# Optimization experiments

Measured on AMD Instinct MI355X. Metric: run time of the kernel, lower is better.

## Reference

```python
import jax, jax.numpy as jnp
import numpy as np

B, HEADS, SCALES, POINTS, HIDDEN = 1, 8, 4, 4, 192
HEAD_DIM = HIDDEN // HEADS
OFFSET_SCALE = 0.35
EPS = 1e-5


def conv1x1(x, W, b=None):
    # x: [B,C,D,H,W], W: [O,C]
    y = jnp.einsum('bcdhw,oc->bodhw', x, W)
    if b is not None:
        y = y + b[None, :, None, None, None]
    return y


def base_grid(D, H, W, dtype):
    z = jnp.linspace(-1.0, 1.0, D, dtype=dtype)
    y = jnp.linspace(-1.0, 1.0, H, dtype=dtype)
    x = jnp.linspace(-1.0, 1.0, W, dtype=dtype)
    zz, yy, xx = jnp.meshgrid(z, y, x, indexing='ij')
    return jnp.stack((xx, yy, zz), axis=-1)  # [D,H,W,3] (x,y,z order)


def trilinear_sample(val, grid):
    # val: [BH,C,Dv,Hv,Wv]; grid: [BH,N,3] normalized (x,y,z), align_corners=False, border padding
    BH, C, Dv, Hv, Wv = val.shape
    unnorm = lambda g, s: jnp.clip(((g + 1.0) * s - 1.0) * 0.5, 0.0, s - 1.0)
    ix = unnorm(grid[..., 0], Wv)
    iy = unnorm(grid[..., 1], Hv)
    iz = unnorm(grid[..., 2], Dv)
    x0f, y0f, z0f = jnp.floor(ix), jnp.floor(iy), jnp.floor(iz)
    wx, wy, wz = ix - x0f, iy - y0f, iz - z0f
    x0 = x0f.astype(jnp.int32); x1 = jnp.minimum(x0 + 1, Wv - 1)
    y0 = y0f.astype(jnp.int32); y1 = jnp.minimum(y0 + 1, Hv - 1)
    z0 = z0f.astype(jnp.int32); z1 = jnp.minimum(z0 + 1, Dv - 1)
    vflat = val.reshape(BH, C, Dv * Hv * Wv)
    gather = jax.vmap(lambda v, i: v[:, i])  # -> [BH,C,N]
    def corner(zi, yi, xi):
        return gather(vflat, (zi * Hv + yi) * Wv + xi)
    w = lambda a: a[:, None, :]  # broadcast weight over channel dim
    out = (corner(z0, y0, x0) * w((1 - wz) * (1 - wy) * (1 - wx))
           + corner(z0, y0, x1) * w((1 - wz) * (1 - wy) * wx)
           + corner(z0, y1, x0) * w((1 - wz) * wy * (1 - wx))
           + corner(z0, y1, x1) * w((1 - wz) * wy * wx)
           + corner(z1, y0, x0) * w(wz * (1 - wy) * (1 - wx))
           + corner(z1, y0, x1) * w(wz * (1 - wy) * wx)
           + corner(z1, y1, x0) * w(wz * wy * (1 - wx))
           + corner(z1, y1, x1) * w(wz * wy * wx))
    return out


def fsad_forward(query_feature, values, Wq, Wvs, Woff, boff, Wwt, bwt, Wout, gamma, beta):
    Bq, _, D, H, W = query_feature.shape
    N = D * H * W
    q = conv1x1(query_feature, Wq)
    off = conv1x1(q, Woff, boff).reshape(Bq, HEADS, SCALES, POINTS, 3, D, H, W)
    off = jnp.tanh(off) * OFFSET_SCALE
    aw = conv1x1(q, Wwt, bwt).reshape(Bq, HEADS, SCALES * POINTS, D, H, W)
    aw = jax.nn.softmax(aw, axis=2).reshape(Bq, HEADS, SCALES, POINTS, D, H, W)
    bg = base_grid(D, H, W, q.dtype)  # [D,H,W,3]
    acc = jnp.zeros((Bq, HEADS, HEAD_DIM, D, H, W), q.dtype)
    for s in range(SCALES):
        feat = values[s]
        val = conv1x1(feat, Wvs[s]).reshape(Bq * HEADS, HEAD_DIM, *feat.shape[2:])
        # off[:,:,s]: [B,Hh,P,3,D,H,W] -> grid [B,Hh,P,D,H,W,3]
        grid = bg[None, None, None] + jnp.moveaxis(off[:, :, s], 3, -1)
        grid = grid.reshape(Bq * HEADS, POINTS * N, 3)
        sampled = trilinear_sample(val, grid).reshape(Bq, HEADS, HEAD_DIM, POINTS, D, H, W)
        acc = acc + jnp.einsum('bhcpdyx,bhpdyx->bhcdyx', sampled, aw[:, :, s])
    out = conv1x1(acc.reshape(Bq, HIDDEN, D, H, W), Wout)
    # InstanceNorm3d(affine=True)
    mu = out.mean(axis=(2, 3, 4), keepdims=True)
    var = out.var(axis=(2, 3, 4), keepdims=True)
    out = (out - mu) * jax.lax.rsqrt(var + EPS)
    return out * gamma[None, :, None, None, None] + beta[None, :, None, None, None]


def setup_inputs() -> dict:
    key = jax.random.key(0)
    ks = jax.random.split(key, 16)
    value_channels = [32, 64, 128, 256]
    sizes = [64, 32, 16, 8]
    inp = {
        'query_feature': jax.random.normal(ks[0], (1, 128, 16, 16, 16), jnp.float32),
        'v0': jax.random.normal(ks[1], (1, 32, 64, 64, 64), jnp.float32),
        'v1': jax.random.normal(ks[2], (1, 64, 32, 32, 32), jnp.float32),
        'v2': jax.random.normal(ks[3], (1, 128, 16, 16, 16), jnp.float32),
        'v3': jax.random.normal(ks[4], (1, 256, 8, 8, 8), jnp.float32),
        'Wq': jax.random.normal(ks[5], (HIDDEN, 128), jnp.float32) * 0.05,
        'Wv0': jax.random.normal(ks[6], (HIDDEN, 32), jnp.float32) * 0.05,
        'Wv1': jax.random.normal(ks[7], (HIDDEN, 64), jnp.float32) * 0.05,
        'Wv2': jax.random.normal(ks[8], (HIDDEN, 128), jnp.float32) * 0.05,
        'Wv3': jax.random.normal(ks[9], (HIDDEN, 256), jnp.float32) * 0.05,
        'Woff': jax.random.normal(ks[10], (HEADS * SCALES * POINTS * 3, HIDDEN), jnp.float32) * 0.05,
        'boff': jnp.zeros((HEADS * SCALES * POINTS * 3,), jnp.float32),
        'Wwt': jax.random.normal(ks[11], (HEADS * SCALES * POINTS, HIDDEN), jnp.float32) * 0.05,
        'bwt': jnp.zeros((HEADS * SCALES * POINTS,), jnp.float32),
        'Wout': jax.random.normal(ks[12], (128, HIDDEN), jnp.float32) * 0.05,
        'gamma': jnp.ones((128,), jnp.float32),
        'beta': jnp.zeros((128,), jnp.float32),
    }
    return inp


def reference(query_feature, v0, v1, v2, v3, Wq, Wv0, Wv1, Wv2, Wv3, Woff, boff, Wwt, bwt, Wout, gamma, beta):
    return fsad_forward(query_feature, [v0, v1, v2, v3], Wq, [Wv0, Wv1, Wv2, Wv3], Woff, boff, Wwt, bwt, Wout, gamma, beta)
```

## Files before the change

### kernel.cpp

```cpp
#include <hip/hip_runtime.h>
#include <hip/hip_fp16.h>
#include <cmath>

#define N_Q 4096
#define HEADS 8
#define HEAD_DIM 24
#define HIDDEN 192

__device__ __forceinline__ float4 ld4(const float* p) { return *(const float4*)p; }

__device__ __forceinline__ void fma8h(float* u, float w, const __half* p) {
    uint4 raw = *(const uint4*)p;
    const __half2* h2 = reinterpret_cast<const __half2*>(&raw);
#pragma unroll
    for (int k = 0; k < 4; k++) {
        float2 f = __half22float2(h2[k]);
        u[2 * k]     = fmaf(w, f.x, u[2 * k]);
        u[2 * k + 1] = fmaf(w, f.y, u[2 * k + 1]);
    }
}

__device__ __forceinline__ void corner24(float* acc, float w, const __half* p) {
    fma8h(acc,      w, p);
    fma8h(acc + 8,  w, p + 8);
    fma8h(acc + 16, w, p + 16);
}

__global__ __launch_bounds__(256)
void wcomb_kernel(const float* __restrict__ Woff, const float* __restrict__ Wwt,
                  const float* __restrict__ Wq, float* __restrict__ Wcomb)
{
    int o = blockIdx.x * 2 + (threadIdx.x >> 7);
    int c = threadIdx.x & 127;
    const float* A = (o < 384) ? (Woff + (size_t)o * 192) : (Wwt + (size_t)(o - 384) * 192);
    float s = 0.f;
#pragma unroll 4
    for (int k = 0; k < 192; k++) s = fmaf(A[k], Wq[k * 128 + c], s);
    Wcomb[(size_t)o * 128 + c] = s;
}

template<int C, int OG, int MODE>
__global__ __launch_bounds__(256)
void convT_kernel(const float* __restrict__ W, const float* __restrict__ bias,
                  const float* __restrict__ x, float* __restrict__ y)
{
    __shared__ float xs[C * 64];
    __shared__ float Wl[OG * C];
    int tid = threadIdx.x;
    int n0 = blockIdx.x * 64;
    int og0 = blockIdx.y * OG;
    for (int k = tid; k < C * 64; k += 256) xs[k] = x[(size_t)(k >> 6) * N_Q + n0 + (k & 63)];
    for (int k = tid; k < OG * C; k += 256) Wl[k] = W[(size_t)(og0 + k / C) * C + (k % C)];
    __syncthreads();

    int wv = tid >> 6, lane = tid & 63;
    constexpr int PT = OG / 4;
    float acc[PT];
#pragma unroll
    for (int i = 0; i < PT; i++) acc[i] = 0.f;
    for (int c = 0; c < C; c++) {
        float xv = xs[c * 64 + lane];
#pragma unroll
        for (int i = 0; i < PT; i++)
            acc[i] = fmaf(Wl[(wv * PT + i) * C + c], xv, acc[i]);
    }
#pragma unroll
    for (int i = 0; i < PT; i++) {
        int o = og0 + wv * PT + i;
        float r = acc[i];
        if constexpr (MODE == 1) r = tanhf(r + bias[o]) * 0.35f;
        if constexpr (MODE == 2) r = r + bias[o];
        y[(size_t)o * N_Q + n0 + lane] = r;
    }
}

__global__ __launch_bounds__(256)
void softmax16_kernel(float* __restrict__ aw)
{
    int idx = blockIdx.x * 256 + threadIdx.x;
    int h = idx >> 12;
    int n = idx & 4095;
    float v[16];
    float m = -1e30f;
#pragma unroll
    for (int i = 0; i < 16; i++) { v[i] = aw[(h * 16 + i) * N_Q + n]; m = fmaxf(m, v[i]); }
    float ssum = 0.f;
#pragma unroll
    for (int i = 0; i < 16; i++) { v[i] = __expf(v[i] - m); ssum += v[i]; }
    float inv = 1.0f / ssum;
#pragma unroll
    for (int i = 0; i < 16; i++) aw[(h * 16 + i) * N_Q + n] = v[i] * inv;
}

template<int C, int P>
__global__ __launch_bounds__(256)
void transpose_h_kernel(const float* __restrict__ src, __half* __restrict__ dst, int Nv)
{
    __shared__ float lds[P][C + 1];
    int tid = threadIdx.x;
    int pos0 = blockIdx.x * P;
    for (int k = tid; k < P * C; k += 256) {
        int c = k / P, p = k % P;
        lds[p][c] = src[c * Nv + pos0 + p];
    }
    __syncthreads();
    for (int k = tid; k < P * C; k += 256) {
        int p = k / C, c = k % C;
        dst[(pos0 + p) * C + c] = __float2half(lds[p][c]);
    }
}

template<int C, int OG>
__global__ __launch_bounds__(256)
void valconv_kernel(const float* __restrict__ Wv, const float* __restrict__ v,
                    __half* __restrict__ valT, int Nv)
{
    __shared__ float Wl[OG][C];
    __shared__ __half outs[64 * OG];
    int tid = threadIdx.x;
    int p0 = blockIdx.x * 64;
    int og0 = blockIdx.y * OG;
    for (int k = tid; k < OG * C; k += 256) Wl[k / C][k % C] = Wv[(size_t)(og0 + k / C) * C + (k % C)];
    __syncthreads();

    int osub = tid >> 6;
    int lane = tid & 63;
    constexpr int PT = OG / 4;
    float acc[PT];
#pragma unroll
    for (int i = 0; i < PT; i++) acc[i] = 0.f;
    for (int c = 0; c < C; c++) {
        float vv = v[(size_t)c * Nv + p0 + lane];
#pragma unroll
        for (int i = 0; i < PT; i++)
            acc[i] = fmaf(Wl[osub * PT + i][c], vv, acc[i]);
    }
#pragma unroll
    for (int i = 0; i < PT; i++)
        outs[lane * OG + osub * PT + i] = __float2half(acc[i]);
    __syncthreads();

    unsigned int* dst = (unsigned int*)valT;
    const unsigned int* src = (const unsigned int*)outs;
    constexpr int UPP = OG / 2;
    for (int k = tid; k < 64 * UPP; k += 256) {
        int p = k / UPP, i = k % UPP;
        dst[(size_t)(p0 + p) * (HIDDEN / 2) + (og0 / 2) + i] = src[p * UPP + i];
    }
}

__global__ __launch_bounds__(256)
void sample_kernel(const float* __restrict__ offb, const float* __restrict__ awb,
                   const __half* __restrict__ v0T, const __half* __restrict__ val1T,
                   const __half* __restrict__ val2T, const __half* __restrict__ val3T,
                   const float* __restrict__ Wv0,
                   float* __restrict__ accb)
{
    int tid = threadIdx.x;
    int n = blockIdx.x * 256 + tid;
    int h = blockIdx.y;
    int sp = blockIdx.z;
    int s = sp >> 2, p = sp & 3;

    int wx = n & 15, hy = (n >> 4) & 15, dz = n >> 8;
    const float step = 2.0f / 15.0f;
    float bx = -1.f + wx * step;
    float by = -1.f + hy * step;
    float bz = -1.f + dz * step;

    float acc[HEAD_DIM];
#pragma unroll
    for (int j = 0; j < HEAD_DIM; j++) acc[j] = 0.f;

    int S = 64;
    const __half* srcT = v0T;
    if (s == 1)      { S = 32; srcT = val1T; }
    else if (s == 2) { S = 16; srcT = val2T; }
    else if (s == 3) { S = 8;  srcT = val3T; }
    float fS = (float)S;

    int orow = ((h * 4 + s) * 4 + p) * 3;
    float ox = offb[(orow + 0) * N_Q + n];
    float oy = offb[(orow + 1) * N_Q + n];
    float oz = offb[(orow + 2) * N_Q + n];
    float awv = awb[(h * 16 + s * 4 + p) * N_Q + n];

    float ix = fminf(fmaxf(((bx + ox + 1.f) * fS - 1.f) * 0.5f, 0.f), fS - 1.f);
    float iy = fminf(fmaxf(((by + oy + 1.f) * fS - 1.f) * 0.5f, 0.f), fS - 1.f);
    float iz = fminf(fmaxf(((bz + oz + 1.f) * fS - 1.f) * 0.5f, 0.f), fS - 1.f);

    float x0f = floorf(ix), y0f = floorf(iy), z0f = floorf(iz);
    float fx = ix - x0f, fy = iy - y0f, fz = iz - z0f;
    int x0 = (int)x0f, y0 = (int)y0f, z0 = (int)z0f;
    int x1 = min(x0 + 1, S - 1), y1 = min(y0 + 1, S - 1), z1 = min(z0 + 1, S - 1);

    int r000 = (z0 * S + y0) * S + x0, r001 = (z0 * S + y0) * S + x1;
    int r010 = (z0 * S + y1) * S + x0, r011 = (z0 * S + y1) * S + x1;
    int r100 = (z1 * S + y0) * S + x0, r101 = (z1 * S + y0) * S + x1;
    int r110 = (z1 * S + y1) * S + x0, r111 = (z1 * S + y1) * S + x1;

    float gx1 = fx, gx0 = 1.f - fx;
    float gy1 = fy, gy0 = 1.f - fy;
    float gz1 = fz, gz0 = 1.f - fz;
    float w000 = gz0 * gy0 * gx0 * awv, w001 = gz0 * gy0 * gx1 * awv;
    float w010 = gz0 * gy1 * gx0 * awv, w011 = gz0 * gy1 * gx1 * awv;
    float w100 = gz1 * gy0 * gx0 * awv, w101 = gz1 * gy0 * gx1 * awv;
    float w110 = gz1 * gy1 * gx0 * awv, w111 = gz1 * gy1 * gx1 * awv;

    if (s == 0) {
        const float* Wvh = Wv0 + h * HEAD_DIM * 32;
#pragma unroll
        for (int c8 = 0; c8 < 32; c8 += 8) {
            float u[8] = {0.f, 0.f, 0.f, 0.f, 0.f, 0.f, 0.f, 0.f};
            fma8h(u, w000, srcT + r000 * 32 + c8);
            fma8h(u, w001, srcT + r001 * 32 + c8);
            fma8h(u, w010, srcT + r010 * 32 + c8);
            fma8h(u, w011, srcT + r011 * 32 + c8);
            fma8h(u, w100, srcT + r100 * 32 + c8);
            fma8h(u, w101, srcT + r101 * 32 + c8);
            fma8h(u, w110, srcT + r110 * 32 + c8);
            fma8h(u, w111, srcT + r111 * 32 + c8);
#pragma unroll
            for (int j = 0; j < HEAD_DIM; j++) {
                const float* wp = Wvh + j * 32 + c8;
                float4 wa = ld4(wp), wb = ld4(wp + 4);
                acc[j] = fmaf(wa.x, u[0], fmaf(wa.y, u[1], fmaf(wa.z, u[2], fmaf(wa.w, u[3],
                         fmaf(wb.x, u[4], fmaf(wb.y, u[5], fmaf(wb.z, u[6], fmaf(wb.w, u[7], acc[j]))))))));
            }
        }
    } else {
        const __half* base = srcT + h * HEAD_DIM;
        corner24(acc, w000, base + (size_t)r000 * HIDDEN);
        corner24(acc, w001, base + (size_t)r001 * HIDDEN);
        corner24(acc, w010, base + (size_t)r010 * HIDDEN);
        corner24(acc, w011, base + (size_t)r011 * HIDDEN);
        corner24(acc, w100, base + (size_t)r100 * HIDDEN);
        corner24(acc, w101, base + (size_t)r101 * HIDDEN);
        corner24(acc, w110, base + (size_t)r110 * HIDDEN);
        corner24(acc, w111, base + (size_t)r111 * HIDDEN);
    }

    float* ab = accb + (size_t)sp * HIDDEN * N_Q;
#pragma unroll
    for (int j = 0; j < HEAD_DIM; j++) ab[(h * HEAD_DIM + j) * N_Q + n] = acc[j];
}

__global__ __launch_bounds__(256)
void accsum_kernel(const float* __restrict__ accb, float* __restrict__ accsum)
{
    int i = blockIdx.x * 256 + threadIdx.x;
    const int SB4 = HIDDEN * N_Q / 4;
    const float4* src = (const float4*)accb;
    float4 a = src[i];
#pragma unroll
    for (int sp = 1; sp < 16; sp++) {
        float4 b = src[sp * SB4 + i];
        a.x += b.x; a.y += b.y; a.z += b.z; a.w += b.w;
    }
    ((float4*)accsum)[i] = a;
}

__global__ __launch_bounds__(256)
void inorm_kernel(float* __restrict__ out, const float* __restrict__ gamma,
                  const float* __restrict__ beta)
{
    int o = blockIdx.x;
    int tid = threadIdx.x;
    float s = 0.f, s2 = 0.f;
    for (int n = tid; n < N_Q; n += 256) {
        float v = out[o * N_Q + n];
        s += v; s2 += v * v;
    }
    __shared__ float rs[256], rs2[256];
    rs[tid] = s; rs2[tid] = s2;
    __syncthreads();
    for (int k = 128; k > 0; k >>= 1) {
        if (tid < k) { rs[tid] += rs[tid + k]; rs2[tid] += rs2[tid + k]; }
        __syncthreads();
    }
    float mu = rs[0] * (1.0f / N_Q);
    float var = rs2[0] * (1.0f / N_Q) - mu * mu;
    float rstd = rsqrtf(var + 1e-5f);
    float g = gamma[o] * rstd;
    float b = beta[o] - mu * g;
    for (int n = tid; n < N_Q; n += 256) {
        out[o * N_Q + n] = fmaf(out[o * N_Q + n], g, b);
    }
}

extern "C" void kernel_launch(void* const* d_in, const int* in_sizes, int n_in,
                              void* d_out, int out_size, void* d_ws, size_t ws_size,
                              hipStream_t stream)
{
    const float* qf    = (const float*)d_in[0];
    const float* v0    = (const float*)d_in[1];
    const float* v1    = (const float*)d_in[2];
    const float* v2    = (const float*)d_in[3];
    const float* v3    = (const float*)d_in[4];
    const float* Wq    = (const float*)d_in[5];
    const float* Wv0   = (const float*)d_in[6];
    const float* Wv1   = (const float*)d_in[7];
    const float* Wv2   = (const float*)d_in[8];
    const float* Wv3   = (const float*)d_in[9];
    const float* Woff  = (const float*)d_in[10];
    const float* boff  = (const float*)d_in[11];
    const float* Wwt   = (const float*)d_in[12];
    const float* bwt   = (const float*)d_in[13];
    const float* Wout  = (const float*)d_in[14];
    const float* gamma = (const float*)d_in[15];
    const float* beta  = (const float*)d_in[16];
    float* out = (float*)d_out;

    float* ws     = (float*)d_ws;
    float*  Wcomb  = ws;
    float*  offb   = Wcomb  + 65536;
    float*  awb    = offb   + 1572864;
    __half* v0T    = (__half*)(awb + 524288);
    __half* val1T  = (__half*)((float*)v0T + 4194304);
    __half* val2T  = (__half*)((float*)val1T + 3145728);
    __half* val3T  = (__half*)((float*)val2T + 393216);
    float*  accb   = (float*)val3T + 49152;
    float*  accsum = accb   + 12582912;

    wcomb_kernel<<<256, 256, 0, stream>>>(Woff, Wwt, Wq, Wcomb);
    convT_kernel<128, 32, 1><<<dim3(64, 12), 256, 0, stream>>>(Wcomb, boff, qf, offb);
    convT_kernel<128, 32, 2><<<dim3(64, 4), 256, 0, stream>>>(Wcomb + 384 * 128, bwt, qf, awb);
    softmax16_kernel<<<128, 256, 0, stream>>>(awb);
    transpose_h_kernel<32, 256><<<1024, 256, 0, stream>>>(v0, v0T, 262144);
    valconv_kernel<64, 24><<<dim3(512, 8), 256, 0, stream>>>(Wv1, v1, val1T, 32768);
    valconv_kernel<128, 12><<<dim3(64, 16), 256, 0, stream>>>(Wv2, v2, val2T, 4096);
    valconv_kernel<256, 8><<<dim3(8, 24), 256, 0, stream>>>(Wv3, v3, val3T, 512);
    sample_kernel<<<dim3(16, 8, 16), 256, 0, stream>>>(offb, awb, v0T, val1T, val2T, val3T,
                                                       Wv0, accb);
    accsum_kernel<<<768, 256, 0, stream>>>(accb, accsum);
    convT_kernel<192, 32, 0><<<dim3(64, 4), 256, 0, stream>>>(Wout, nullptr, accsum, out);
    inorm_kernel<<<128, 256, 0, stream>>>(out, gamma, beta);
}
```

Before: 312.8 us.

## Store sampling partials in fp16 and merge conv and valconv launches

The sampling kernel now writes its 16 per-scale/point partial accumulators as fp16 instead of fp32, and the reduction kernel reads them with 8-wide half loads. This halves the largest intermediate buffer's write and read traffic. The offset and weight 1x1 convs become one launch using a combined bias array, and the three value-projection convs become a single launch dispatched by block id, cutting launch overhead. The fp16 partials add rounding error before summation.

```diff
diff --git a/kernel.cpp b/kernel.cpp
--- a/kernel.cpp
+++ b/kernel.cpp
@@ -28,7 +28,9 @@
 
 __global__ __launch_bounds__(256)
 void wcomb_kernel(const float* __restrict__ Woff, const float* __restrict__ Wwt,
-                  const float* __restrict__ Wq, float* __restrict__ Wcomb)
+                  const float* __restrict__ Wq, const float* __restrict__ boff,
+                  const float* __restrict__ bwt, float* __restrict__ Wcomb,
+                  float* __restrict__ biasc)
 {
     int o = blockIdx.x * 2 + (threadIdx.x >> 7);
     int c = threadIdx.x & 127;
@@ -37,6 +39,7 @@
 #pragma unroll 4
     for (int k = 0; k < 192; k++) s = fmaf(A[k], Wq[k * 128 + c], s);
     Wcomb[(size_t)o * 128 + c] = s;
+    if (c == 0) biasc[o] = (o < 384) ? boff[o] : bwt[o - 384];
 }
 
 template<int C, int OG, int MODE>
@@ -68,8 +71,9 @@
     for (int i = 0; i < PT; i++) {
         int o = og0 + wv * PT + i;
         float r = acc[i];
-        if constexpr (MODE == 1) r = tanhf(r + bias[o]) * 0.35f;
-        if constexpr (MODE == 2) r = r + bias[o];
+        if constexpr (MODE == 3) {
+            r = (o < 384) ? tanhf(r + bias[o]) * 0.35f : r + bias[o];
+        }
         y[(size_t)o * N_Q + n0 + lane] = r;
     }
 }
@@ -111,15 +115,15 @@
 }
 
 template<int C, int OG>
-__global__ __launch_bounds__(256)
-void valconv_kernel(const float* __restrict__ Wv, const float* __restrict__ v,
-                    __half* __restrict__ valT, int Nv)
+__device__ __forceinline__ void valconv_body(const float* __restrict__ Wv,
+                                             const float* __restrict__ v,
+                                             __half* __restrict__ valT, int Nv,
+                                             int bx, int by, int tid)
 {
     __shared__ float Wl[OG][C];
     __shared__ __half outs[64 * OG];
-    int tid = threadIdx.x;
-    int p0 = blockIdx.x * 64;
-    int og0 = blockIdx.y * OG;
+    int p0 = bx * 64;
+    int og0 = by * OG;
     for (int k = tid; k < OG * C; k += 256) Wl[k / C][k % C] = Wv[(size_t)(og0 + k / C) * C + (k % C)];
     __syncthreads();
 
@@ -150,16 +154,39 @@
 }
 
 __global__ __launch_bounds__(256)
+void valconv_all_kernel(const float* __restrict__ Wv1, const float* __restrict__ v1,
+                        __half* __restrict__ val1T,
+                        const float* __restrict__ Wv2, const float* __restrict__ v2,
+                        __half* __restrict__ val2T,
+                        const float* __restrict__ Wv3, const float* __restrict__ v3,
+                        __half* __restrict__ val3T)
+{
+    int id = blockIdx.x;
+    int tid = threadIdx.x;
+    if (id < 4096) {
+        valconv_body<64, 24>(Wv1, v1, val1T, 32768, id & 511, id >> 9, tid);
+    } else if (id < 5120) {
+        int i2 = id - 4096;
+        valconv_body<128, 12>(Wv2, v2, val2T, 4096, i2 & 63, i2 >> 6, tid);
+    } else {
+        int i3 = id - 5120;
+        valconv_body<256, 8>(Wv3, v3, val3T, 512, i3 & 7, i3 >> 3, tid);
+    }
+}
+
+__global__ __launch_bounds__(256)
 void sample_kernel(const float* __restrict__ offb, const float* __restrict__ awb,
                    const __half* __restrict__ v0T, const __half* __restrict__ val1T,
                    const __half* __restrict__ val2T, const __half* __restrict__ val3T,
                    const float* __restrict__ Wv0,
-                   float* __restrict__ accb)
-{
-    int tid = threadIdx.x;
-    int n = blockIdx.x * 256 + tid;
-    int h = blockIdx.y;
-    int sp = blockIdx.z;
+                   __half* __restrict__ accb)
+{
+    int tid = threadIdx.x;
+    int id = blockIdx.x;
+    int t = id & 15;
+    int h = (id >> 4) & 7;
+    int sp = id >> 7;
+    int n = t * 256 + tid;
     int s = sp >> 2, p = sp & 3;
 
     int wx = n & 15, hy = (n >> 4) & 15, dz = n >> 8;
@@ -240,24 +267,31 @@
         corner24(acc, w111, base + (size_t)r111 * HIDDEN);
     }
 
-    float* ab = accb + (size_t)sp * HIDDEN * N_Q;
-#pragma unroll
-    for (int j = 0; j < HEAD_DIM; j++) ab[(h * HEAD_DIM + j) * N_Q + n] = acc[j];
-}
-
-__global__ __launch_bounds__(256)
-void accsum_kernel(const float* __restrict__ accb, float* __restrict__ accsum)
+    __half* ab = accb + (size_t)sp * HIDDEN * N_Q;
+#pragma unroll
+    for (int j = 0; j < HEAD_DIM; j++) ab[(h * HEAD_DIM + j) * N_Q + n] = __float2half(acc[j]);
+}
+
+__global__ __launch_bounds__(256)
+void accsum_kernel(const __half* __restrict__ accb, float* __restrict__ accsum)
 {
     int i = blockIdx.x * 256 + threadIdx.x;
-    const int SB4 = HIDDEN * N_Q / 4;
-    const float4* src = (const float4*)accb;
-    float4 a = src[i];
-#pragma unroll
-    for (int sp = 1; sp < 16; sp++) {
-        float4 b = src[sp * SB4 + i];
-        a.x += b.x; a.y += b.y; a.z += b.z; a.w += b.w;
-    }
-    ((float4*)accsum)[i] = a;
+    const int SB8 = HIDDEN * N_Q / 8;
+    const uint4* src = (const uint4*)accb;
+    float a[8] = {0.f, 0.f, 0.f, 0.f, 0.f, 0.f, 0.f, 0.f};
+#pragma unroll
+    for (int sp = 0; sp < 16; sp++) {
+        uint4 r = src[sp * SB8 + i];
+        const __half2* h2 = (const __half2*)&r;
+#pragma unroll
+        for (int k = 0; k < 4; k++) {
+            float2 f = __half22float2(h2[k]);
+            a[2 * k] += f.x; a[2 * k + 1] += f.y;
+        }
+    }
+    float4* dst = (float4*)accsum;
+    dst[i * 2]     = make_float4(a[0], a[1], a[2], a[3]);
+    dst[i * 2 + 1] = make_float4(a[4], a[5], a[6], a[7]);
 }
 
 __global__ __launch_bounds__(256)
@@ -313,26 +347,23 @@
 
     float* ws     = (float*)d_ws;
     float*  Wcomb  = ws;
-    float*  offb   = Wcomb  + 65536;
+    float*  biasc  = Wcomb  + 65536;
+    float*  offb   = biasc  + 512;
     float*  awb    = offb   + 1572864;
     __half* v0T    = (__half*)(awb + 524288);
     __half* val1T  = (__half*)((float*)v0T + 4194304);
     __half* val2T  = (__half*)((float*)val1T + 3145728);
     __half* val3T  = (__half*)((float*)val2T + 393216);
-    float*  accb   = (float*)val3T + 49152;
-    float*  accsum = accb   + 12582912;
-
-    wcomb_kernel<<<256, 256, 0, stream>>>(Woff, Wwt, Wq, Wcomb);
-    convT_kernel<128, 32, 1><<<dim3(64, 12), 256, 0, stream>>>(Wcomb, boff, qf, offb);
-    convT_kernel<128, 32, 2><<<dim3(64, 4), 256, 0, stream>>>(Wcomb + 384 * 128, bwt, qf, awb);
+    __half* accb   = (__half*)((float*)val3T + 49152);
+    float*  accsum = (float*)accb + 6291456;
+
+    wcomb_kernel<<<256, 256, 0, stream>>>(Woff, Wwt, Wq, boff, bwt, Wcomb, biasc);
+    convT_kernel<128, 32, 3><<<dim3(64, 16), 256, 0, stream>>>(Wcomb, biasc, qf, offb);
     softmax16_kernel<<<128, 256, 0, stream>>>(awb);
     transpose_h_kernel<32, 256><<<1024, 256, 0, stream>>>(v0, v0T, 262144);
-    valconv_kernel<64, 24><<<dim3(512, 8), 256, 0, stream>>>(Wv1, v1, val1T, 32768);
-    valconv_kernel<128, 12><<<dim3(64, 16), 256, 0, stream>>>(Wv2, v2, val2T, 4096);
-    valconv_kernel<256, 8><<<dim3(8, 24), 256, 0, stream>>>(Wv3, v3, val3T, 512);
-    sample_kernel<<<dim3(16, 8, 16), 256, 0, stream>>>(offb, awb, v0T, val1T, val2T, val3T,
-                                                       Wv0, accb);
-    accsum_kernel<<<768, 256, 0, stream>>>(accb, accsum);
+    valconv_all_kernel<<<5312, 256, 0, stream>>>(Wv1, v1, val1T, Wv2, v2, val2T, Wv3, v3, val3T);
+    sample_kernel<<<2048, 256, 0, stream>>>(offb, awb, v0T, val1T, val2T, val3T, Wv0, accb);
+    accsum_kernel<<<384, 256, 0, stream>>>(accb, accsum);
     convT_kernel<192, 32, 0><<<dim3(64, 4), 256, 0, stream>>>(Wout, nullptr, accsum, out);
     inorm_kernel<<<128, 256, 0, stream>>>(out, gamma, beta);
 }
```

Result: faster. 281.8 us (-9.9%).
